# Performance work log

Hardware: AMD Instinct MI355X
Metric: run time of the kernel (lower is better)

The kernel has to match this reference:

```python
import jax, jax.numpy as jnp
import numpy as np

B, Mc, Mt, E, VOCAB, NREL, HOPS = 16, 2048, 4096, 512, 32000, 69, 2


def setup_inputs() -> dict:
    key = jax.random.key(0)
    ks = jax.random.split(key, 10)
    s = 1.0 / np.sqrt(E)
    return {
        "concept_table": jax.random.normal(ks[0], (VOCAB, E), jnp.float32) * 0.02,
        "relation_table": jax.random.normal(ks[1], (NREL, E), jnp.float32) * 0.02,
        "W_s": jax.random.uniform(ks[2], (HOPS, E, E), jnp.float32, -s, s),
        "W_n": jax.random.uniform(ks[3], (HOPS, E, E), jnp.float32, -s, s),
        "W_r": jax.random.uniform(ks[4], (HOPS, E, E), jnp.float32, -s, s),
        "concept_ids": jax.random.randint(ks[5], (B, Mc), 0, VOCAB, jnp.int32),
        "relation_ids": jax.random.randint(ks[6], (B, Mt), 0, NREL, jnp.int32),
        "head_idx": jax.random.randint(ks[7], (B, Mt), 0, Mc, jnp.int32),
        "tail_idx": jax.random.randint(ks[8], (B, Mt), 0, Mc, jnp.int32),
        "triple_labels": jax.random.randint(ks[9], (B, Mt), -1, 2, jnp.int32),
    }


def reference(concept_table, relation_table, W_s, W_n, W_r,
              concept_ids, relation_ids, head_idx, tail_idx, triple_labels):
    b, mt = head_idx.shape
    mc = concept_ids.shape[1]
    h = concept_table[concept_ids]          # B x Mc x E
    r = relation_table[relation_ids]        # B x Mt x E
    valid = (triple_labels != -1)
    mask = valid[..., None].astype(h.dtype)  # B x Mt x 1
    cnt = valid.astype(h.dtype)              # B x Mt
    bidx = jnp.arange(b)[:, None]
    num_hops = W_s.shape[0]
    for l in range(num_hops):
        rm = r * mask
        o_h = jnp.take_along_axis(h, head_idx[..., None], axis=1) * mask
        o_t = jnp.take_along_axis(h, tail_idx[..., None], axis=1) * mask
        upd = jnp.zeros_like(h)
        upd = upd.at[bidx, tail_idx].add(o_h - rm)   # messages head->tail
        upd = upd.at[bidx, head_idx].add(o_t - rm)   # messages tail->head
        count = jnp.zeros((b, mc), h.dtype)
        count = count.at[bidx, tail_idx].add(cnt).at[bidx, head_idx].add(cnt)
        h = jax.nn.relu(h @ W_s[l].T + (upd @ W_n[l].T) / jnp.clip(count, 1.0)[..., None])
        r = r @ W_r[l].T
    head_repr = jnp.take_along_axis(h, head_idx[..., None], axis=1)  # B x Mt x E
    tail_repr = jnp.take_along_axis(h, tail_idx[..., None], axis=1)
    return jnp.concatenate((head_repr, r, tail_repr), axis=-1)       # B x Mt x 3E
```

## Files before the change

kernel.cpp:

```cpp
#include <hip/hip_runtime.h>
#include <stdint.h>

#define B_   16
#define MC   2048
#define MT   4096
#define E_   512
#define NRELS 69

typedef __attribute__((ext_vector_type(8))) short bf16x8;
typedef __attribute__((ext_vector_type(4))) float floatx4;

typedef __attribute__((address_space(1))) const void gvoid_t;
typedef __attribute__((address_space(3))) void lvoid_t;

__device__ inline float b2f(ushort u) {
  union { uint32_t i; float f; } x; x.i = ((uint32_t)u) << 16; return x.f;
}
__device__ inline ushort f2b(float f) {
  union { float f; uint32_t u; } v; v.f = f;
  uint32_t r = (v.u + 0x7fffu + ((v.u >> 16) & 1u)) >> 16;
  return (ushort)r;
}

__device__ inline void gl2lds(const ushort* g, ushort* l) {
  __builtin_amdgcn_global_load_lds((gvoid_t*)g, (lvoid_t*)l, 16, 0, 0);
}

__device__ inline int block_detect(const ushort* ct) {
  __shared__ int sflag;
  if (threadIdx.x == 0) sflag = 0;
  __syncthreads();
  int bad = 0;
  for (int j = threadIdx.x; j < 1024; j += 256) {
    int e = (ct[j] >> 7) & 0xFF;
    if (e >= 0xC0) bad = 1;
  }
  if (bad) sflag = 1;
  __syncthreads();
  return sflag;
}

__device__ inline void cvt8(const void* src, ushort* dst, int c, int flag) {
  if (flag) {
    const float* s = (const float*)src + (size_t)c * 8;
    float4 a = *(const float4*)s, b = *(const float4*)(s + 4);
    uint32_t p0 = (uint32_t)f2b(a.x) | ((uint32_t)f2b(a.y) << 16);
    uint32_t p1 = (uint32_t)f2b(a.z) | ((uint32_t)f2b(a.w) << 16);
    uint32_t p2 = (uint32_t)f2b(b.x) | ((uint32_t)f2b(b.y) << 16);
    uint32_t p3 = (uint32_t)f2b(b.z) | ((uint32_t)f2b(b.w) << 16);
    *(uint4*)(dst + (size_t)c * 8) = make_uint4(p0, p1, p2, p3);
  } else {
    *(uint4*)(dst + (size_t)c * 8) = *(const uint4*)((const ushort*)src + (size_t)c * 8);
  }
}

#define NW8 (2 * E_ * E_ / 8)
#define NR8 (NRELS * E_ / 8)
#define NGH (B_ * MC * 64)
#define NCT (B_ * MT)
#define SEC1 (NW8)
#define SEC2 (2 * NW8)
#define SEC3 (3 * NW8)
#define SEC4 (SEC3 + NR8)
#define SEC5 (SEC4 + NGH)
#define STOT (SEC5 + NCT)

__global__ void preproc_k(const void* __restrict__ ct, const void* __restrict__ rt,
                          const void* __restrict__ Ws, const void* __restrict__ Wn,
                          const void* __restrict__ Wr,
                          const int* __restrict__ cids, const int* __restrict__ heads,
                          const int* __restrict__ tails, const int* __restrict__ labels,
                          ushort* __restrict__ Wsb, ushort* __restrict__ Wnb,
                          ushort* __restrict__ Wrb, ushort* __restrict__ rtab0,
                          ushort* __restrict__ h0, int* __restrict__ cnt) {
  int flag = block_detect((const ushort*)ct);
  int c = blockIdx.x * 256 + threadIdx.x;
  if (c >= STOT) return;
  if (c < SEC3) {
    if (c < SEC1)       cvt8(Ws, Wsb, c, flag);
    else if (c < SEC2)  cvt8(Wn, Wnb, c - SEC1, flag);
    else                cvt8(Wr, Wrb, c - SEC2, flag);
  } else if (c < SEC4) {
    cvt8(rt, rtab0, c - SEC3, flag);
  } else if (c < SEC5) {
    int g = c - SEC4;
    int row = g >> 6, col = (g & 63) << 3;
    int src = cids[row];
    if (flag) {
      const float* s = (const float*)ct + (size_t)src * E_ + col;
      float4 a = *(const float4*)s, b = *(const float4*)(s + 4);
      uint32_t p0 = (uint32_t)f2b(a.x) | ((uint32_t)f2b(a.y) << 16);
      uint32_t p1 = (uint32_t)f2b(a.z) | ((uint32_t)f2b(a.w) << 16);
      uint32_t p2 = (uint32_t)f2b(b.x) | ((uint32_t)f2b(b.y) << 16);
      uint32_t p3 = (uint32_t)f2b(b.z) | ((uint32_t)f2b(b.w) << 16);
      *(uint4*)(h0 + (size_t)row * E_ + col) = make_uint4(p0, p1, p2, p3);
    } else {
      *(uint4*)(h0 + (size_t)row * E_ + col) =
          *(const uint4*)((const ushort*)ct + (size_t)src * E_ + col);
    }
  } else {
    int t = c - SEC5;
    if (labels[t] != -1) {
      int b = t >> 12;
      atomicAdd(&cnt[b * MC + heads[t]], 1);
      atomicAdd(&cnt[b * MC + tails[t]], 1);
    }
  }
}

__global__ void scan_inv_k(const int* __restrict__ cnt, int* __restrict__ offs,
                           float* __restrict__ inv) {
  __shared__ int part[1024];
  int tid = threadIdx.x;
  const int CH = (B_ * MC) / 1024;
  int base = tid * CH, s = 0;
  for (int i = 0; i < CH; ++i) s += cnt[base + i];
  part[tid] = s;
  __syncthreads();
  for (int off = 1; off < 1024; off <<= 1) {
    int v = (tid >= off) ? part[tid - off] : 0;
    __syncthreads();
    part[tid] += v;
    __syncthreads();
  }
  int run = (tid == 0) ? 0 : part[tid - 1];
  for (int i = 0; i < CH; ++i) {
    int cc = cnt[base + i];
    offs[base + i] = run;
    inv[base + i] = 1.0f / (float)(cc > 1 ? cc : 1);
    run += cc;
  }
  if (tid == 1023) offs[B_ * MC] = run;
}

__global__ void fill_k(const int* __restrict__ head, const int* __restrict__ tail,
                       const int* __restrict__ rid, const int* __restrict__ labels,
                       const int* __restrict__ offs, int* __restrict__ cursor,
                       int* __restrict__ edges) {
  int t = blockIdx.x * blockDim.x + threadIdx.x;
  if (t >= B_ * MT) return;
  if (labels[t] == -1) return;
  int b = t >> 12;
  int hb = b * MC + head[t], tb = b * MC + tail[t];
  int r = rid[t];
  int p = atomicAdd(&cursor[tb], 1);
  edges[offs[tb] + p] = head[t] | (r << 16);
  p = atomicAdd(&cursor[hb], 1);
  edges[offs[hb] + p] = tail[t] | (r << 16);
}

__global__ void gather_msg_k(const ushort* __restrict__ h, const ushort* __restrict__ rtab,
                             const int* __restrict__ edges, const int* __restrict__ offs,
                             const float* __restrict__ inv, ushort* __restrict__ updb) {
  int row = blockIdx.x * 4 + (threadIdx.x >> 6);
  int lane = threadIdx.x & 63;
  int col = lane << 3;
  int beg = offs[row], end = offs[row + 1];
  int b = row >> 11;
  float acc[8];
#pragma unroll
  for (int i = 0; i < 8; ++i) acc[i] = 0.f;
  const ushort* hbase = h + (size_t)b * MC * E_ + col;
  for (int e = beg; e < end; ++e) {
    int ent = edges[e];
    int other = ent & 0xffff, rid = ent >> 16;
    uint4 vh = *(const uint4*)(hbase + (size_t)other * E_);
    uint4 vr = *(const uint4*)(rtab + (size_t)rid * E_ + col);
    uint32_t wh[4] = {vh.x, vh.y, vh.z, vh.w};
    uint32_t wr[4] = {vr.x, vr.y, vr.z, vr.w};
#pragma unroll
    for (int i = 0; i < 4; ++i) {
      acc[2 * i]     += b2f((ushort)(wh[i] & 0xffff)) - b2f((ushort)(wr[i] & 0xffff));
      acc[2 * i + 1] += b2f((ushort)(wh[i] >> 16))    - b2f((ushort)(wr[i] >> 16));
    }
  }
  float s = inv[row];
  uint32_t p[4];
#pragma unroll
  for (int i = 0; i < 4; ++i)
    p[i] = (uint32_t)f2b(acc[2 * i] * s) | ((uint32_t)f2b(acc[2 * i + 1] * s) << 16);
  *(uint4*)(updb + (size_t)row * E_ + col) = make_uint4(p[0], p[1], p[2], p[3]);
}

__global__ void rel2_gemm_k(const ushort* __restrict__ rtab0, const ushort* __restrict__ Wr,
                            ushort* __restrict__ rtab1, ushort* __restrict__ rtab2) {
  __shared__ float arow[E_];
  int n = blockIdx.x;
  int tid = threadIdx.x;
  for (int k = tid; k < E_; k += 256) arow[k] = b2f(rtab0[n * E_ + k]);
  __syncthreads();
  for (int hp = 0; hp < 2; ++hp) {
    const ushort* W = Wr + (size_t)hp * E_ * E_;
    int ca = tid, cb = tid + 256;
    float acc0 = 0.f, acc1 = 0.f;
    const ushort* wa = W + (size_t)ca * E_;
    const ushort* wb = W + (size_t)cb * E_;
    for (int k = 0; k < E_; k += 8) {
      uint4 w8a = *(const uint4*)(wa + k);
      uint4 w8b = *(const uint4*)(wb + k);
      uint32_t va[4] = {w8a.x, w8a.y, w8a.z, w8a.w};
      uint32_t vb[4] = {w8b.x, w8b.y, w8b.z, w8b.w};
#pragma unroll
      for (int i = 0; i < 4; ++i) {
        float a0 = arow[k + 2 * i], a1 = arow[k + 2 * i + 1];
        acc0 += a0 * b2f((ushort)(va[i] & 0xffff)) + a1 * b2f((ushort)(va[i] >> 16));
        acc1 += a0 * b2f((ushort)(vb[i] & 0xffff)) + a1 * b2f((ushort)(vb[i] >> 16));
      }
    }
    __syncthreads();
    ushort ra = f2b(acc0), rb = f2b(acc1);
    ushort* o = hp ? rtab2 : rtab1;
    o[n * E_ + ca] = ra;
    o[n * E_ + cb] = rb;
    arow[ca] = b2f(ra);
    arow[cb] = b2f(rb);
    __syncthreads();
  }
}

#define BM 128
#define BN 128
#define BK 64

__global__ __launch_bounds__(256) void gemm_h_k(
    const ushort* __restrict__ A0, const ushort* __restrict__ W0,
    const ushort* __restrict__ A1, const ushort* __restrict__ W1,
    ushort* __restrict__ C) {
  const int N = E_, K = E_;
  __shared__ __align__(16) ushort As[BM * BK];
  __shared__ __align__(16) ushort Bs[BN * BK];
  int nbn = N / BN;
  int bm = blockIdx.x / nbn, bn = blockIdx.x % nbn;
  int tid = threadIdx.x;
  int lane = tid & 63, wid = tid >> 6;
  int wm = (wid >> 1) * 64, wn = (wid & 1) * 64;
  int lrow = lane & 15, lq = lane >> 4;

  floatx4 acc[4][4];
#pragma unroll
  for (int i = 0; i < 4; ++i)
#pragma unroll
    for (int j = 0; j < 4; ++j) acc[i][j] = (floatx4)(0.0f);

  for (int pass = 0; pass < 2; ++pass) {
    const ushort* Am = pass ? A1 : A0;
    const ushort* Wm = pass ? W1 : W0;
    for (int k0 = 0; k0 < K; k0 += BK) {
#pragma unroll
      for (int i = 0; i < 4; ++i) {
        int c = tid + i * 256;
        int row = c >> 3, col = (c & 7) << 3;
        gl2lds(Am + (size_t)(bm * BM + row) * K + k0 + col, As + row * BK + col);
      }
#pragma unroll
      for (int i = 0; i < 4; ++i) {
        int c = tid + i * 256;
        int row = c >> 3, col = (c & 7) << 3;
        gl2lds(Wm + (size_t)(bn * BN + row) * K + k0 + col, Bs + row * BK + col);
      }
      __syncthreads();
#pragma unroll
      for (int kk = 0; kk < BK; kk += 32) {
        bf16x8 af[4], bfr[4];
#pragma unroll
        for (int mi = 0; mi < 4; ++mi)
          af[mi] = *(const bf16x8*)(As + (wm + mi * 16 + lrow) * BK + kk + lq * 8);
#pragma unroll
        for (int ni = 0; ni < 4; ++ni)
          bfr[ni] = *(const bf16x8*)(Bs + (wn + ni * 16 + lrow) * BK + kk + lq * 8);
#pragma unroll
        for (int mi = 0; mi < 4; ++mi)
#pragma unroll
          for (int ni = 0; ni < 4; ++ni)
            acc[mi][ni] = __builtin_amdgcn_mfma_f32_16x16x32_bf16(af[mi], bfr[ni], acc[mi][ni], 0, 0, 0);
      }
      __syncthreads();
    }
  }
#pragma unroll
  for (int mi = 0; mi < 4; ++mi)
#pragma unroll
    for (int ni = 0; ni < 4; ++ni)
#pragma unroll
      for (int rg = 0; rg < 4; ++rg) {
        int row = bm * BM + wm + mi * 16 + lq * 4 + rg;
        int col = bn * BN + wn + ni * 16 + lrow;
        C[(size_t)row * N + col] = f2b(fmaxf(acc[mi][ni][rg], 0.0f));
      }
}

__global__ void out_k(const ushort* __restrict__ h, const ushort* __restrict__ rtab,
                      const int* __restrict__ rid,
                      const int* __restrict__ head, const int* __restrict__ tail,
                      void* __restrict__ out, const ushort* __restrict__ ctab) {
  int flag = block_detect(ctab);
  int gid = blockIdx.x * blockDim.x + threadIdx.x;
  int t = gid / 192;
  if (t >= B_ * MT) return;
  int sc = gid - t * 192;
  int sec = sc >> 6;
  int col = (sc & 63) << 3;
  int b = t >> 12;
  const ushort* src;
  if (sec == 0)      src = h + (size_t)(b * MC + head[t]) * E_ + col;
  else if (sec == 1) src = rtab + (size_t)rid[t] * E_ + col;
  else               src = h + (size_t)(b * MC + tail[t]) * E_ + col;
  size_t o = (size_t)t * 1536 + sec * 512 + col;
  if (flag) {
    float* fo = (float*)out + o;
    uint4 v = *(const uint4*)src;
    uint32_t w[4] = {v.x, v.y, v.z, v.w};
    float4 f0, f1;
    f0.x = b2f((ushort)(w[0] & 0xffff)); f0.y = b2f((ushort)(w[0] >> 16));
    f0.z = b2f((ushort)(w[1] & 0xffff)); f0.w = b2f((ushort)(w[1] >> 16));
    f1.x = b2f((ushort)(w[2] & 0xffff)); f1.y = b2f((ushort)(w[2] >> 16));
    f1.z = b2f((ushort)(w[3] & 0xffff)); f1.w = b2f((ushort)(w[3] >> 16));
    *(float4*)fo = f0;
    *(float4*)(fo + 4) = f1;
  } else {
    *(uint4*)((ushort*)out + o) = *(const uint4*)src;
  }
}

extern "C" void kernel_launch(void* const* d_in, const int* in_sizes, int n_in,
                              void* d_out, int out_size, void* d_ws, size_t ws_size,
                              hipStream_t stream) {
  const void* concept_table  = d_in[0];
  const void* relation_table = d_in[1];
  const void* W_s = d_in[2];
  const void* W_n = d_in[3];
  const void* W_r = d_in[4];
  const int* concept_ids  = (const int*)d_in[5];
  const int* relation_ids = (const int*)d_in[6];
  const int* head_idx = (const int*)d_in[7];
  const int* tail_idx = (const int*)d_in[8];
  const int* labels   = (const int*)d_in[9];

  char* ws = (char*)d_ws;
  size_t off = 0;
  auto alloc = [&](size_t bytes) {
    char* p = ws + off;
    off += (bytes + 255) & ~(size_t)255;
    return p;
  };
  ushort* h_a    = (ushort*)alloc((size_t)B_ * MC * E_ * 2);
  ushort* h_b    = (ushort*)alloc((size_t)B_ * MC * E_ * 2);
  int*    cnt    = (int*)   alloc((size_t)B_ * MC * 4);
  float*  inv    = (float*) alloc((size_t)B_ * MC * 4);
  int*    offs   = (int*)   alloc(((size_t)B_ * MC + 1) * 4);
  int*    cursor = (int*)   alloc((size_t)B_ * MC * 4);
  int*    edges  = (int*)   alloc((size_t)2 * B_ * MT * 4);
  ushort* Wsb    = (ushort*)alloc((size_t)2 * E_ * E_ * 2);
  ushort* Wnb    = (ushort*)alloc((size_t)2 * E_ * E_ * 2);
  ushort* Wrb    = (ushort*)alloc((size_t)2 * E_ * E_ * 2);
  ushort* rtab0  = (ushort*)alloc((size_t)NRELS * E_ * 2);
  ushort* rtab1  = (ushort*)alloc((size_t)NRELS * E_ * 2);
  ushort* rtab2  = (ushort*)alloc((size_t)NRELS * E_ * 2);
  ushort* updb   = (ushort*)d_out;

  hipMemsetAsync(cnt, 0, (size_t)B_ * MC * 4, stream);
  hipMemsetAsync(cursor, 0, (size_t)B_ * MC * 4, stream);

  preproc_k<<<(STOT + 255) / 256, 256, 0, stream>>>(
      concept_table, relation_table, W_s, W_n, W_r,
      concept_ids, head_idx, tail_idx, labels,
      Wsb, Wnb, Wrb, rtab0, h_a, cnt);

  scan_inv_k<<<1, 1024, 0, stream>>>(cnt, offs, inv);
  fill_k<<<(B_ * MT + 255) / 256, 256, 0, stream>>>(head_idx, tail_idx, relation_ids, labels,
                                                    offs, cursor, edges);

  rel2_gemm_k<<<NRELS, 256, 0, stream>>>(rtab0, Wrb, rtab1, rtab2);

  gather_msg_k<<<B_ * MC / 4, 256, 0, stream>>>(h_a, rtab0, edges, offs, inv, updb);
  gemm_h_k<<<(B_ * MC / BM) * (E_ / BN), 256, 0, stream>>>(h_a, Wsb, updb, Wnb, h_b);

  gather_msg_k<<<B_ * MC / 4, 256, 0, stream>>>(h_b, rtab1, edges, offs, inv, updb);
  gemm_h_k<<<(B_ * MC / BM) * (E_ / BN), 256, 0, stream>>>(h_b, Wsb + (size_t)E_ * E_, updb,
                                                           Wnb + (size_t)E_ * E_, h_a);

  out_k<<<(B_ * MT * 192 + 255) / 256, 256, 0, stream>>>(h_a, rtab2, relation_ids,
                                                         head_idx, tail_idx, d_out,
                                                         (const ushort*)concept_table);
}
```

Before: 718.4 us.

## Merge edge fill with relation GEMM, widen output stores, add nontemporal hints

Fuses the CSR edge-fill kernel and the small relation-table GEMM into one launch, with the first blocks doing the GEMM and the rest filling edges. The output kernel now has each thread handle 16 elements and writes with nontemporal stores. Preprocessing loads become nontemporal, and gather_msg prefetches the next edge index. The goal is fewer launches and less cache pollution on the output write, which is the largest transfer, at the cost of more registers per thread in out_k.

```diff
diff --git a/kernel.cpp b/kernel.cpp
--- a/kernel.cpp
+++ b/kernel.cpp
@@ -9,6 +9,8 @@
 
 typedef __attribute__((ext_vector_type(8))) short bf16x8;
 typedef __attribute__((ext_vector_type(4))) float floatx4;
+typedef __attribute__((ext_vector_type(4))) float f32x4;
+typedef __attribute__((ext_vector_type(4))) unsigned int u32x4;
 
 typedef __attribute__((address_space(1))) const void gvoid_t;
 typedef __attribute__((address_space(3))) void lvoid_t;
@@ -43,14 +45,17 @@
 __device__ inline void cvt8(const void* src, ushort* dst, int c, int flag) {
   if (flag) {
     const float* s = (const float*)src + (size_t)c * 8;
-    float4 a = *(const float4*)s, b = *(const float4*)(s + 4);
-    uint32_t p0 = (uint32_t)f2b(a.x) | ((uint32_t)f2b(a.y) << 16);
-    uint32_t p1 = (uint32_t)f2b(a.z) | ((uint32_t)f2b(a.w) << 16);
-    uint32_t p2 = (uint32_t)f2b(b.x) | ((uint32_t)f2b(b.y) << 16);
-    uint32_t p3 = (uint32_t)f2b(b.z) | ((uint32_t)f2b(b.w) << 16);
-    *(uint4*)(dst + (size_t)c * 8) = make_uint4(p0, p1, p2, p3);
+    f32x4 a = __builtin_nontemporal_load((const f32x4*)s);
+    f32x4 b = __builtin_nontemporal_load((const f32x4*)(s + 4));
+    u32x4 p;
+    p.x = (uint32_t)f2b(a.x) | ((uint32_t)f2b(a.y) << 16);
+    p.y = (uint32_t)f2b(a.z) | ((uint32_t)f2b(a.w) << 16);
+    p.z = (uint32_t)f2b(b.x) | ((uint32_t)f2b(b.y) << 16);
+    p.w = (uint32_t)f2b(b.z) | ((uint32_t)f2b(b.w) << 16);
+    *(u32x4*)(dst + (size_t)c * 8) = p;
   } else {
-    *(uint4*)(dst + (size_t)c * 8) = *(const uint4*)((const ushort*)src + (size_t)c * 8);
+    u32x4 v = __builtin_nontemporal_load((const u32x4*)((const ushort*)src + (size_t)c * 8));
+    *(u32x4*)(dst + (size_t)c * 8) = v;
   }
 }
 
@@ -88,15 +93,18 @@
     int src = cids[row];
     if (flag) {
       const float* s = (const float*)ct + (size_t)src * E_ + col;
-      float4 a = *(const float4*)s, b = *(const float4*)(s + 4);
-      uint32_t p0 = (uint32_t)f2b(a.x) | ((uint32_t)f2b(a.y) << 16);
-      uint32_t p1 = (uint32_t)f2b(a.z) | ((uint32_t)f2b(a.w) << 16);
-      uint32_t p2 = (uint32_t)f2b(b.x) | ((uint32_t)f2b(b.y) << 16);
-      uint32_t p3 = (uint32_t)f2b(b.z) | ((uint32_t)f2b(b.w) << 16);
-      *(uint4*)(h0 + (size_t)row * E_ + col) = make_uint4(p0, p1, p2, p3);
+      f32x4 a = __builtin_nontemporal_load((const f32x4*)s);
+      f32x4 b = __builtin_nontemporal_load((const f32x4*)(s + 4));
+      u32x4 p;
+      p.x = (uint32_t)f2b(a.x) | ((uint32_t)f2b(a.y) << 16);
+      p.y = (uint32_t)f2b(a.z) | ((uint32_t)f2b(a.w) << 16);
+      p.z = (uint32_t)f2b(b.x) | ((uint32_t)f2b(b.y) << 16);
+      p.w = (uint32_t)f2b(b.z) | ((uint32_t)f2b(b.w) << 16);
+      *(u32x4*)(h0 + (size_t)row * E_ + col) = p;
     } else {
-      *(uint4*)(h0 + (size_t)row * E_ + col) =
-          *(const uint4*)((const ushort*)ct + (size_t)src * E_ + col);
+      u32x4 v = __builtin_nontemporal_load(
+          (const u32x4*)((const ushort*)ct + (size_t)src * E_ + col));
+      *(u32x4*)(h0 + (size_t)row * E_ + col) = v;
     }
   } else {
     int t = c - SEC5;
@@ -133,20 +141,57 @@
   if (tid == 1023) offs[B_ * MC] = run;
 }
 
-__global__ void fill_k(const int* __restrict__ head, const int* __restrict__ tail,
-                       const int* __restrict__ rid, const int* __restrict__ labels,
-                       const int* __restrict__ offs, int* __restrict__ cursor,
-                       int* __restrict__ edges) {
-  int t = blockIdx.x * blockDim.x + threadIdx.x;
-  if (t >= B_ * MT) return;
-  if (labels[t] == -1) return;
-  int b = t >> 12;
-  int hb = b * MC + head[t], tb = b * MC + tail[t];
-  int r = rid[t];
-  int p = atomicAdd(&cursor[tb], 1);
-  edges[offs[tb] + p] = head[t] | (r << 16);
-  p = atomicAdd(&cursor[hb], 1);
-  edges[offs[hb] + p] = tail[t] | (r << 16);
+__global__ void mid_k(const ushort* __restrict__ rtab0, const ushort* __restrict__ Wr,
+                      ushort* __restrict__ rtab1, ushort* __restrict__ rtab2,
+                      const int* __restrict__ head, const int* __restrict__ tail,
+                      const int* __restrict__ rid, const int* __restrict__ labels,
+                      const int* __restrict__ offs, int* __restrict__ cursor,
+                      int* __restrict__ edges) {
+  __shared__ float arow[E_];
+  int tid = threadIdx.x;
+  if (blockIdx.x < NRELS) {
+    int n = blockIdx.x;
+    for (int k = tid; k < E_; k += 256) arow[k] = b2f(rtab0[n * E_ + k]);
+    __syncthreads();
+    for (int hp = 0; hp < 2; ++hp) {
+      const ushort* W = Wr + (size_t)hp * E_ * E_;
+      int ca = tid, cb = tid + 256;
+      float acc0 = 0.f, acc1 = 0.f;
+      const ushort* wa = W + (size_t)ca * E_;
+      const ushort* wb = W + (size_t)cb * E_;
+      for (int k = 0; k < E_; k += 8) {
+        u32x4 w8a = *(const u32x4*)(wa + k);
+        u32x4 w8b = *(const u32x4*)(wb + k);
+        uint32_t va[4] = {w8a.x, w8a.y, w8a.z, w8a.w};
+        uint32_t vb[4] = {w8b.x, w8b.y, w8b.z, w8b.w};
+#pragma unroll
+        for (int i = 0; i < 4; ++i) {
+          float a0 = arow[k + 2 * i], a1 = arow[k + 2 * i + 1];
+          acc0 += a0 * b2f((ushort)(va[i] & 0xffff)) + a1 * b2f((ushort)(va[i] >> 16));
+          acc1 += a0 * b2f((ushort)(vb[i] & 0xffff)) + a1 * b2f((ushort)(vb[i] >> 16));
+        }
+      }
+      __syncthreads();
+      ushort ra = f2b(acc0), rb = f2b(acc1);
+      ushort* o = hp ? rtab2 : rtab1;
+      o[n * E_ + ca] = ra;
+      o[n * E_ + cb] = rb;
+      arow[ca] = b2f(ra);
+      arow[cb] = b2f(rb);
+      __syncthreads();
+    }
+  } else {
+    int t = (blockIdx.x - NRELS) * 256 + tid;
+    if (t >= B_ * MT) return;
+    if (labels[t] == -1) return;
+    int b = t >> 12;
+    int hb = b * MC + head[t], tb = b * MC + tail[t];
+    int r = rid[t];
+    int p = atomicAdd(&cursor[tb], 1);
+    edges[offs[tb] + p] = head[t] | (r << 16);
+    p = atomicAdd(&cursor[hb], 1);
+    edges[offs[hb] + p] = tail[t] | (r << 16);
+  }
 }
 
 __global__ void gather_msg_k(const ushort* __restrict__ h, const ushort* __restrict__ rtab,
@@ -161,61 +206,28 @@
 #pragma unroll
   for (int i = 0; i < 8; ++i) acc[i] = 0.f;
   const ushort* hbase = h + (size_t)b * MC * E_ + col;
+  int ent = (beg < end) ? edges[beg] : 0;
   for (int e = beg; e < end; ++e) {
-    int ent = edges[e];
-    int other = ent & 0xffff, rid = ent >> 16;
-    uint4 vh = *(const uint4*)(hbase + (size_t)other * E_);
-    uint4 vr = *(const uint4*)(rtab + (size_t)rid * E_ + col);
-    uint32_t wh[4] = {vh.x, vh.y, vh.z, vh.w};
-    uint32_t wr[4] = {vr.x, vr.y, vr.z, vr.w};
+    int nxt = (e + 1 < end) ? edges[e + 1] : 0;
+    int other = ent & 0xffff, rr = ent >> 16;
+    u32x4 wh = *(const u32x4*)(hbase + (size_t)other * E_);
+    u32x4 wr = *(const u32x4*)(rtab + (size_t)rr * E_ + col);
+    uint32_t hh[4] = {wh.x, wh.y, wh.z, wh.w};
+    uint32_t rv[4] = {wr.x, wr.y, wr.z, wr.w};
 #pragma unroll
     for (int i = 0; i < 4; ++i) {
-      acc[2 * i]     += b2f((ushort)(wh[i] & 0xffff)) - b2f((ushort)(wr[i] & 0xffff));
-      acc[2 * i + 1] += b2f((ushort)(wh[i] >> 16))    - b2f((ushort)(wr[i] >> 16));
-    }
+      acc[2 * i]     += b2f((ushort)(hh[i] & 0xffff)) - b2f((ushort)(rv[i] & 0xffff));
+      acc[2 * i + 1] += b2f((ushort)(hh[i] >> 16))    - b2f((ushort)(rv[i] >> 16));
+    }
+    ent = nxt;
   }
   float s = inv[row];
-  uint32_t p[4];
-#pragma unroll
-  for (int i = 0; i < 4; ++i)
-    p[i] = (uint32_t)f2b(acc[2 * i] * s) | ((uint32_t)f2b(acc[2 * i + 1] * s) << 16);
-  *(uint4*)(updb + (size_t)row * E_ + col) = make_uint4(p[0], p[1], p[2], p[3]);
-}
-
-__global__ void rel2_gemm_k(const ushort* __restrict__ rtab0, const ushort* __restrict__ Wr,
-                            ushort* __restrict__ rtab1, ushort* __restrict__ rtab2) {
-  __shared__ float arow[E_];
-  int n = blockIdx.x;
-  int tid = threadIdx.x;
-  for (int k = tid; k < E_; k += 256) arow[k] = b2f(rtab0[n * E_ + k]);
-  __syncthreads();
-  for (int hp = 0; hp < 2; ++hp) {
-    const ushort* W = Wr + (size_t)hp * E_ * E_;
-    int ca = tid, cb = tid + 256;
-    float acc0 = 0.f, acc1 = 0.f;
-    const ushort* wa = W + (size_t)ca * E_;
-    const ushort* wb = W + (size_t)cb * E_;
-    for (int k = 0; k < E_; k += 8) {
-      uint4 w8a = *(const uint4*)(wa + k);
-      uint4 w8b = *(const uint4*)(wb + k);
-      uint32_t va[4] = {w8a.x, w8a.y, w8a.z, w8a.w};
-      uint32_t vb[4] = {w8b.x, w8b.y, w8b.z, w8b.w};
-#pragma unroll
-      for (int i = 0; i < 4; ++i) {
-        float a0 = arow[k + 2 * i], a1 = arow[k + 2 * i + 1];
-        acc0 += a0 * b2f((ushort)(va[i] & 0xffff)) + a1 * b2f((ushort)(va[i] >> 16));
-        acc1 += a0 * b2f((ushort)(vb[i] & 0xffff)) + a1 * b2f((ushort)(vb[i] >> 16));
-      }
-    }
-    __syncthreads();
-    ushort ra = f2b(acc0), rb = f2b(acc1);
-    ushort* o = hp ? rtab2 : rtab1;
-    o[n * E_ + ca] = ra;
-    o[n * E_ + cb] = rb;
-    arow[ca] = b2f(ra);
-    arow[cb] = b2f(rb);
-    __syncthreads();
-  }
+  u32x4 p;
+  p.x = (uint32_t)f2b(acc[0] * s) | ((uint32_t)f2b(acc[1] * s) << 16);
+  p.y = (uint32_t)f2b(acc[2] * s) | ((uint32_t)f2b(acc[3] * s) << 16);
+  p.z = (uint32_t)f2b(acc[4] * s) | ((uint32_t)f2b(acc[5] * s) << 16);
+  p.w = (uint32_t)f2b(acc[6] * s) | ((uint32_t)f2b(acc[7] * s) << 16);
+  *(u32x4*)(updb + (size_t)row * E_ + col) = p;
 }
 
 #define BM 128
@@ -294,31 +306,36 @@
                       const int* __restrict__ head, const int* __restrict__ tail,
                       void* __restrict__ out, const ushort* __restrict__ ctab) {
   int flag = block_detect(ctab);
-  int gid = blockIdx.x * blockDim.x + threadIdx.x;
-  int t = gid / 192;
+  int gp = blockIdx.x * blockDim.x + threadIdx.x;
+  int t = gp / 96;
   if (t >= B_ * MT) return;
-  int sc = gid - t * 192;
-  int sec = sc >> 6;
-  int col = (sc & 63) << 3;
+  int sp = gp - t * 96;
+  int sec = sp >> 5;
+  int col = (sp & 31) << 4;
   int b = t >> 12;
   const ushort* src;
   if (sec == 0)      src = h + (size_t)(b * MC + head[t]) * E_ + col;
   else if (sec == 1) src = rtab + (size_t)rid[t] * E_ + col;
   else               src = h + (size_t)(b * MC + tail[t]) * E_ + col;
+  u32x4 v0 = *(const u32x4*)src;
+  u32x4 v1 = *(const u32x4*)(src + 8);
   size_t o = (size_t)t * 1536 + sec * 512 + col;
   if (flag) {
     float* fo = (float*)out + o;
-    uint4 v = *(const uint4*)src;
-    uint32_t w[4] = {v.x, v.y, v.z, v.w};
-    float4 f0, f1;
-    f0.x = b2f((ushort)(w[0] & 0xffff)); f0.y = b2f((ushort)(w[0] >> 16));
-    f0.z = b2f((ushort)(w[1] & 0xffff)); f0.w = b2f((ushort)(w[1] >> 16));
-    f1.x = b2f((ushort)(w[2] & 0xffff)); f1.y = b2f((ushort)(w[2] >> 16));
-    f1.z = b2f((ushort)(w[3] & 0xffff)); f1.w = b2f((ushort)(w[3] >> 16));
-    *(float4*)fo = f0;
-    *(float4*)(fo + 4) = f1;
+    uint32_t w[8] = {v0.x, v0.y, v0.z, v0.w, v1.x, v1.y, v1.z, v1.w};
+#pragma unroll
+    for (int i = 0; i < 4; ++i) {
+      f32x4 f;
+      f.x = b2f((ushort)(w[2 * i] & 0xffff));
+      f.y = b2f((ushort)(w[2 * i] >> 16));
+      f.z = b2f((ushort)(w[2 * i + 1] & 0xffff));
+      f.w = b2f((ushort)(w[2 * i + 1] >> 16));
+      __builtin_nontemporal_store(f, (f32x4*)fo + i);
+    }
   } else {
-    *(uint4*)((ushort*)out + o) = *(const uint4*)src;
+    ushort* po = (ushort*)out + o;
+    __builtin_nontemporal_store(v0, (u32x4*)po);
+    __builtin_nontemporal_store(v1, (u32x4*)po + 1);
   }
 }
 
@@ -367,10 +384,10 @@
       Wsb, Wnb, Wrb, rtab0, h_a, cnt);
 
   scan_inv_k<<<1, 1024, 0, stream>>>(cnt, offs, inv);
-  fill_k<<<(B_ * MT + 255) / 256, 256, 0, stream>>>(head_idx, tail_idx, relation_ids, labels,
-                                                    offs, cursor, edges);
-
-  rel2_gemm_k<<<NRELS, 256, 0, stream>>>(rtab0, Wrb, rtab1, rtab2);
+
+  mid_k<<<NRELS + (B_ * MT + 255) / 256, 256, 0, stream>>>(
+      rtab0, Wrb, rtab1, rtab2,
+      head_idx, tail_idx, relation_ids, labels, offs, cursor, edges);
 
   gather_msg_k<<<B_ * MC / 4, 256, 0, stream>>>(h_a, rtab0, edges, offs, inv, updb);
   gemm_h_k<<<(B_ * MC / BM) * (E_ / BN), 256, 0, stream>>>(h_a, Wsb, updb, Wnb, h_b);
@@ -379,7 +396,7 @@
   gemm_h_k<<<(B_ * MC / BM) * (E_ / BN), 256, 0, stream>>>(h_b, Wsb + (size_t)E_ * E_, updb,
                                                            Wnb + (size_t)E_ * E_, h_a);
 
-  out_k<<<(B_ * MT * 192 + 255) / 256, 256, 0, stream>>>(h_a, rtab2, relation_ids,
-                                                         head_idx, tail_idx, d_out,
-                                                         (const ushort*)concept_table);
-}
+  out_k<<<(B_ * MT * 96 + 255) / 256, 256, 0, stream>>>(h_a, rtab2, relation_ids,
+                                                        head_idx, tail_idx, d_out,
+                                                        (const ushort*)concept_table);
+}
```

New measurement: 1.069 ms. 1.49x slower.
